# Kernel optimization log

Hardware: AMD Instinct MI355X
Metric: run time of the kernel (lower is better)

Reference implementation:

```python
import jax, jax.numpy as jnp
import numpy as np

N = 100000
E = 1600000
D_IN = 128
D_OUT = 128


def setup_inputs() -> dict:
    key = jax.random.key(0)
    k1, k2, k3, k4 = jax.random.split(key, 4)
    x = jax.random.normal(k1, (N, D_IN), dtype=jnp.float32)
    edge_index = jax.random.randint(k2, (2, E), 0, N, dtype=jnp.int64)
    edge_weight = jax.random.uniform(k3, (E,), dtype=jnp.float32)
    # PyG Linear (glorot) weight stored as [in, out] so that xw = x @ weight
    weight = jax.random.normal(k4, (D_IN, D_OUT), dtype=jnp.float32) * (1.0 / np.sqrt(D_IN))
    bias = jnp.zeros((D_OUT,), dtype=jnp.float32)
    prelu_a = jnp.full((1,), 0.25, dtype=jnp.float32)  # nn.PReLU default
    return {"x": x, "edge_index": edge_index, "edge_weight": edge_weight,
            "weight": weight, "bias": bias, "prelu_a": prelu_a}


def _gcn_forward(x, edge_index, edge_weight, weight, bias, prelu_a):
    n = x.shape[0]
    # Linear transform first (PyG GCNConv applies lin before propagate)
    xw = x @ weight  # [N, D_OUT]

    # gcn_norm: add self-loops with weight 1.0
    loop = jnp.arange(n, dtype=edge_index.dtype)
    row = jnp.concatenate([edge_index[0], loop])  # source
    col = jnp.concatenate([edge_index[1], loop])  # target
    ew = jnp.concatenate([edge_weight, jnp.ones((n,), dtype=edge_weight.dtype)])

    # symmetric normalization: deg computed at targets
    deg = jax.ops.segment_sum(ew, col, num_segments=n)  # [N]
    dinv = jnp.where(deg > 0, jax.lax.rsqrt(deg), 0.0)
    norm = dinv[row] * ew * dinv[col]  # [E+N]

    # gather-scale-scatter aggregation
    msgs = norm[:, None] * xw[row]  # [E+N, D_OUT]
    out = jax.ops.segment_sum(msgs, col, num_segments=n) + bias

    # PReLU (single shared slope)
    return jnp.where(out >= 0, out, prelu_a[0] * out)


def reference(x, edge_index, edge_weight, weight, bias, prelu_a):
    return _gcn_forward(x, edge_index, edge_weight, weight, bias, prelu_a)
```

## Files before the change

kernel.cpp:

```cpp
#include <hip/hip_runtime.h>
#include <hip/hip_bf16.h>

#define D 128
#define NBMAX 512
#define CURPAD 16

typedef __attribute__((ext_vector_type(8))) short bf16x8;
typedef __attribute__((ext_vector_type(4))) float f32x4;

__device__ inline unsigned short f2bf(float f) {
    unsigned u = __float_as_uint(f);
    u = (u + 0x7FFFu + ((u >> 16) & 1u)) >> 16;
    return (unsigned short)u;
}
__device__ inline float bf2f_lo(unsigned u) { return __uint_as_float(u << 16); }
__device__ inline float bf2f_hi(unsigned u) { return __uint_as_float(u & 0xFFFF0000u); }

__global__ void zero_int(int* __restrict__ p, int n) {
    int i = blockIdx.x * 256 + threadIdx.x;
    if (i < n) p[i] = 0;
}

__global__ __launch_bounds__(256) void bucket_count(const int* __restrict__ coli,
                                                    int* __restrict__ bcount, int NB, int E) {
    __shared__ int hist[NBMAX];
    int tid = threadIdx.x;
    for (int i = tid; i < NBMAX; i += 256) hist[i] = 0;
    __syncthreads();
    int base = blockIdx.x * 4096;
    #pragma unroll
    for (int j = 0; j < 16; ++j) {
        int e = base + j * 256 + tid;
        if (e < E) atomicAdd(&hist[coli[e] >> 8], 1);
    }
    __syncthreads();
    for (int i = tid; i < NB; i += 256) {
        int c = hist[i];
        if (c) atomicAdd(&bcount[i * CURPAD], c);
    }
}

__global__ __launch_bounds__(512) void bucket_scan(const int* __restrict__ bcount,
                                                   int* __restrict__ bbase,
                                                   int* __restrict__ bcursor, int NB) {
    __shared__ int sd[512];
    int tid = threadIdx.x;
    int v = (tid < NB) ? bcount[tid * CURPAD] : 0;
    sd[tid] = v; __syncthreads();
    for (int off = 1; off < 512; off <<= 1) {
        int t = (tid >= off) ? sd[tid - off] : 0;
        __syncthreads(); sd[tid] += t; __syncthreads();
    }
    int excl = sd[tid] - v;
    if (tid < NB) { bbase[tid] = excl; bcursor[tid * CURPAD] = excl; }
    if (tid == NB - 1) bbase[NB] = excl + v;
}

__global__ __launch_bounds__(1024) void phase1(const int* __restrict__ rowi,
                                               const int* __restrict__ coli,
                                               const float* __restrict__ ew,
                                               int* __restrict__ bcursor,
                                               int2* __restrict__ tmp, int E) {
    __shared__ int hist[NBMAX];
    __shared__ int runbase[NBMAX];
    int tid = threadIdx.x;
    for (int i = tid; i < NBMAX; i += 1024) hist[i] = 0;
    __syncthreads();
    int base = blockIdx.x * 8192;
    int col[8], row[8], rank[8]; float w[8];
    #pragma unroll
    for (int j = 0; j < 8; ++j) {
        int e = base + j * 1024 + tid;
        if (e < E) {
            col[j] = coli[e]; row[j] = rowi[e]; w[j] = ew[e];
            rank[j] = atomicAdd(&hist[col[j] >> 8], 1);
        }
    }
    __syncthreads();
    for (int i = tid; i < NBMAX; i += 1024) {
        int c = hist[i];
        runbase[i] = c ? atomicAdd(&bcursor[i * CURPAD], c) : 0;
    }
    __syncthreads();
    #pragma unroll
    for (int j = 0; j < 8; ++j) {
        int e = base + j * 1024 + tid;
        if (e < E) {
            int b = col[j] >> 8;
            int pos = runbase[b] + rank[j];
            tmp[pos] = make_int2(((col[j] & 255) << 24) | row[j], __float_as_int(w[j]));
        }
    }
}

__global__ __launch_bounds__(256) void phase2(const int2* __restrict__ tmp,
                                              const int* __restrict__ bbase,
                                              int* __restrict__ rowptr, int* __restrict__ cnt,
                                              float* __restrict__ dinv,
                                              int2* __restrict__ sorted, int N) {
    __shared__ unsigned int cnt_s[256];
    __shared__ unsigned long long deg_s[256];
    __shared__ int scan_s[256];
    __shared__ int cur[256];
    int tid = threadIdx.x;
    cnt_s[tid] = 0; deg_s[tid] = 0;
    __syncthreads();
    int start = bbase[blockIdx.x];
    int end   = bbase[blockIdx.x + 1];
    for (int e = start + tid; e < end; e += 256) {
        int2 v = tmp[e];
        unsigned coff = ((unsigned)v.x) >> 24;
        atomicAdd(&cnt_s[coff], 1u);
        unsigned long long fx =
            (unsigned long long)(__int_as_float(v.y) * 1048576.0f + 0.5f);
        atomicAdd(&deg_s[coff], fx);
    }
    __syncthreads();
    int v0 = (int)cnt_s[tid];
    scan_s[tid] = v0; __syncthreads();
    for (int off = 1; off < 256; off <<= 1) {
        int t = (tid >= off) ? scan_s[tid - off] : 0;
        __syncthreads(); scan_s[tid] += t; __syncthreads();
    }
    int excl = scan_s[tid] - v0;
    int node = blockIdx.x * 256 + tid;
    if (node < N) {
        rowptr[node] = start + excl;
        cnt[node] = v0;
        float deg = 1.0f + (float)((double)deg_s[tid] * (1.0 / 1048576.0));
        dinv[node] = rsqrtf(deg);
    }
    cur[tid] = start + excl;
    __syncthreads();
    for (int e = start + tid; e < end; e += 256) {
        int2 v = tmp[e];
        unsigned coff = ((unsigned)v.x) >> 24;
        int pos = atomicAdd(&cur[coff], 1);
        sorted[pos] = make_int2(v.x & 0xFFFFFF, v.y);
    }
}

__global__ __launch_bounds__(256) void gemm_mfma(const float* __restrict__ x,
                                                 const float* __restrict__ W,
                                                 unsigned short* __restrict__ xw, int N) {
    __shared__ bf16x8 smW[2048];
    int tid = threadIdx.x;

    for (int idx = tid; idx < 2048; idx += 256) {
        int tile = idx >> 6;
        int ln   = idx & 63;
        int kt   = tile >> 3;
        int ct   = tile & 7;
        int k0   = kt * 32 + (ln >> 4) * 8;
        int nn   = ct * 16 + (ln & 15);
        bf16x8 v;
        #pragma unroll
        for (int j = 0; j < 8; ++j) v[j] = (short)f2bf(W[(k0 + j) * D + nn]);
        smW[idx] = v;
    }
    __syncthreads();

    int wid  = tid >> 6;
    int lane = tid & 63;
    int quad = lane >> 4;
    int m16  = lane & 15;
    int row0 = blockIdx.x * 64 + wid * 16;
    int row  = row0 + m16;

    f32x4 acc[8];
    #pragma unroll
    for (int ct = 0; ct < 8; ++ct) acc[ct] = (f32x4){0.f, 0.f, 0.f, 0.f};

    #pragma unroll
    for (int kt = 0; kt < 4; ++kt) {
        bf16x8 a;
        if (row < N) {
            const float* xp = x + (size_t)row * D + kt * 32 + quad * 8;
            float4 u0 = *(const float4*)xp;
            float4 u1 = *(const float4*)(xp + 4);
            a[0] = (short)f2bf(u0.x); a[1] = (short)f2bf(u0.y);
            a[2] = (short)f2bf(u0.z); a[3] = (short)f2bf(u0.w);
            a[4] = (short)f2bf(u1.x); a[5] = (short)f2bf(u1.y);
            a[6] = (short)f2bf(u1.z); a[7] = (short)f2bf(u1.w);
        } else {
            #pragma unroll
            for (int j = 0; j < 8; ++j) a[j] = 0;
        }
        #pragma unroll
        for (int ct = 0; ct < 8; ++ct) {
            acc[ct] = __builtin_amdgcn_mfma_f32_16x16x32_bf16(
                a, smW[(kt * 8 + ct) * 64 + lane], acc[ct], 0, 0, 0);
        }
    }

    int rq = row0 + quad * 4;
    #pragma unroll
    for (int i = 0; i < 4; ++i) {
        int r = rq + i;
        if (r < N) {
            unsigned short* op = xw + (size_t)r * D + m16;
            #pragma unroll
            for (int ct = 0; ct < 8; ++ct) op[ct * 16] = f2bf(acc[ct][i]);
        }
    }
}

__global__ __launch_bounds__(256) void aggregate(const unsigned short* __restrict__ xw,
                                                 const float* __restrict__ dinv,
                                                 const int* __restrict__ rowptr,
                                                 const int* __restrict__ cnt,
                                                 const int2* __restrict__ sorted,
                                                 const float* __restrict__ bias,
                                                 const float* __restrict__ prelu_a,
                                                 float* __restrict__ out, int N) {
    int wid  = threadIdx.x >> 6;
    int lane = threadIdx.x & 63;
    int n = blockIdx.x * 4 + wid;
    if (n >= N) return;
    int d0 = lane * 2;
    float di = dinv[n];
    unsigned xs = *(const unsigned*)(xw + (size_t)n * D + d0);
    float ax = di * bf2f_lo(xs);
    float ay = di * bf2f_hi(xs);
    int s = rowptr[n];
    int cn = cnt[n];
    for (int base = 0; base < cn; base += 64) {
        int rem = cn - base;
        int m = rem < 64 ? rem : 64;
        int rsrc = 0; float wv = 0.f;
        if (lane < rem) {
            int2 er = sorted[s + base + lane];
            rsrc = er.x;
            wv = dinv[er.x] * __int_as_float(er.y);
        }
        int j = 0;
        for (; j + 4 <= m; j += 4) {
            int   r0 = __shfl(rsrc, j + 0), r1 = __shfl(rsrc, j + 1);
            int   r2 = __shfl(rsrc, j + 2), r3 = __shfl(rsrc, j + 3);
            float w0 = __shfl(wv, j + 0), w1 = __shfl(wv, j + 1);
            float w2 = __shfl(wv, j + 2), w3 = __shfl(wv, j + 3);
            unsigned v0 = *(const unsigned*)(xw + (size_t)r0 * D + d0);
            unsigned v1 = *(const unsigned*)(xw + (size_t)r1 * D + d0);
            unsigned v2 = *(const unsigned*)(xw + (size_t)r2 * D + d0);
            unsigned v3 = *(const unsigned*)(xw + (size_t)r3 * D + d0);
            ax = fmaf(w0, bf2f_lo(v0), ax); ay = fmaf(w0, bf2f_hi(v0), ay);
            ax = fmaf(w1, bf2f_lo(v1), ax); ay = fmaf(w1, bf2f_hi(v1), ay);
            ax = fmaf(w2, bf2f_lo(v2), ax); ay = fmaf(w2, bf2f_hi(v2), ay);
            ax = fmaf(w3, bf2f_lo(v3), ax); ay = fmaf(w3, bf2f_hi(v3), ay);
        }
        for (; j < m; ++j) {
            int   r = __shfl(rsrc, j);
            float w = __shfl(wv, j);
            unsigned v = *(const unsigned*)(xw + (size_t)r * D + d0);
            ax = fmaf(w, bf2f_lo(v), ax);
            ay = fmaf(w, bf2f_hi(v), ay);
        }
    }
    float a = prelu_a[0];
    float2 bv = *(const float2*)(bias + d0);
    float ox = fmaf(di, ax, bv.x);
    float oy = fmaf(di, ay, bv.y);
    ox = (ox >= 0.f) ? ox : a * ox;
    oy = (oy >= 0.f) ? oy : a * oy;
    *(float2*)(out + (size_t)n * D + d0) = make_float2(ox, oy);
}

extern "C" void kernel_launch(void* const* d_in, const int* in_sizes, int n_in,
                              void* d_out, int out_size, void* d_ws, size_t ws_size,
                              hipStream_t stream) {
    const float* x       = (const float*)d_in[0];
    const int*   ei      = (const int*)d_in[1];
    const float* ew      = (const float*)d_in[2];
    const float* W       = (const float*)d_in[3];
    const float* bias    = (const float*)d_in[4];
    const float* prelu_a = (const float*)d_in[5];
    float* out = (float*)d_out;

    int N = in_sizes[0] / D;
    int E = in_sizes[2];
    const int* rowi = ei;
    const int* coli = ei + E;
    int NB = (N + 255) >> 8;

    char* ws = (char*)d_ws;
    size_t o = 0;
    int2*  tmp    = (int2*)(ws + o); o += (size_t)E * 8;
    int2*  sorted = (int2*)(ws + o); o += (size_t)E * 8;
    unsigned short* xw = (unsigned short*)(ws + o); o += (size_t)N * D * 2;
    int* bcount  = (int*)(ws + o); o += (size_t)NB * CURPAD * 4;
    int* bcursor = (int*)(ws + o); o += (size_t)NB * CURPAD * 4;
    int* bbase   = (int*)(ws + o); o += ((size_t)NB + 1) * 4;
    o = (o + 255) & ~(size_t)255;
    int* rowptr  = (int*)(ws + o); o += (size_t)N * 4;
    int* cnt     = (int*)(ws + o); o += (size_t)N * 4;
    float* dinv  = (float*)(ws + o); o += (size_t)N * 4;

    zero_int<<<(NB * CURPAD + 255) / 256, 256, 0, stream>>>(bcount, NB * CURPAD);
    bucket_count<<<(E + 4095) / 4096, 256, 0, stream>>>(coli, bcount, NB, E);
    bucket_scan<<<1, 512, 0, stream>>>(bcount, bbase, bcursor, NB);
    phase1<<<(E + 8191) / 8192, 1024, 0, stream>>>(rowi, coli, ew, bcursor, tmp, E);
    phase2<<<NB, 256, 0, stream>>>(tmp, bbase, rowptr, cnt, dinv, sorted, N);
    gemm_mfma<<<(N + 63) / 64, 256, 0, stream>>>(x, W, xw, N);
    aggregate<<<(N + 3) / 4, 256, 0, stream>>>(xw, dinv, rowptr, cnt, sorted, bias, prelu_a, out, N);
}
```

Measured before the change: 246.8 us.

## Prescale xw by dinv in GEMM, vectorize aggregate gather across edge groups

The source-side dinv scaling moves into the GEMM epilogue, so the aggregate no longer does a per-edge dinv gather. The aggregate now has 16 lanes each load 16 bytes of a row, with four edges in flight per wavefront, a software-prefetched next load, and a cross-group shuffle reduction at the end. W is converted to bf16 MFMA layout once by a separate tiny kernel and read from global memory instead of being rebuilt in LDS by every GEMM block. The trade-offs are an extra reduction step, 48 of 64 lanes idle in the epilogue, and B-operand reads that now go through cache instead of LDS.

```diff
diff --git a/kernel.cpp b/kernel.cpp
--- a/kernel.cpp
+++ b/kernel.cpp
@@ -140,13 +140,10 @@
     }
 }
 
-__global__ __launch_bounds__(256) void gemm_mfma(const float* __restrict__ x,
-                                                 const float* __restrict__ W,
-                                                 unsigned short* __restrict__ xw, int N) {
-    __shared__ bf16x8 smW[2048];
-    int tid = threadIdx.x;
-
-    for (int idx = tid; idx < 2048; idx += 256) {
+__global__ __launch_bounds__(256) void prep_W(const float* __restrict__ W,
+                                              bf16x8* __restrict__ gW) {
+    int t = threadIdx.x;
+    for (int idx = t; idx < 2048; idx += 256) {
         int tile = idx >> 6;
         int ln   = idx & 63;
         int kt   = tile >> 3;
@@ -156,10 +153,15 @@
         bf16x8 v;
         #pragma unroll
         for (int j = 0; j < 8; ++j) v[j] = (short)f2bf(W[(k0 + j) * D + nn]);
-        smW[idx] = v;
-    }
-    __syncthreads();
-
+        gW[idx] = v;
+    }
+}
+
+__global__ __launch_bounds__(256) void gemm_mfma(const float* __restrict__ x,
+                                                 const bf16x8* __restrict__ gW,
+                                                 const float* __restrict__ dinv,
+                                                 unsigned short* __restrict__ yw, int N) {
+    int tid  = threadIdx.x;
     int wid  = tid >> 6;
     int lane = tid & 63;
     int quad = lane >> 4;
@@ -189,7 +191,7 @@
         #pragma unroll
         for (int ct = 0; ct < 8; ++ct) {
             acc[ct] = __builtin_amdgcn_mfma_f32_16x16x32_bf16(
-                a, smW[(kt * 8 + ct) * 64 + lane], acc[ct], 0, 0, 0);
+                a, gW[(kt * 8 + ct) * 64 + lane], acc[ct], 0, 0, 0);
         }
     }
 
@@ -198,14 +200,15 @@
     for (int i = 0; i < 4; ++i) {
         int r = rq + i;
         if (r < N) {
-            unsigned short* op = xw + (size_t)r * D + m16;
+            float sc = dinv[r];
+            unsigned short* op = yw + (size_t)r * D + m16;
             #pragma unroll
-            for (int ct = 0; ct < 8; ++ct) op[ct * 16] = f2bf(acc[ct][i]);
-        }
-    }
-}
-
-__global__ __launch_bounds__(256) void aggregate(const unsigned short* __restrict__ xw,
+            for (int ct = 0; ct < 8; ++ct) op[ct * 16] = f2bf(sc * acc[ct][i]);
+        }
+    }
+}
+
+__global__ __launch_bounds__(256) void aggregate(const unsigned short* __restrict__ yw,
                                                  const float* __restrict__ dinv,
                                                  const int* __restrict__ rowptr,
                                                  const int* __restrict__ cnt,
@@ -217,52 +220,74 @@
     int lane = threadIdx.x & 63;
     int n = blockIdx.x * 4 + wid;
     if (n >= N) return;
-    int d0 = lane * 2;
-    float di = dinv[n];
-    unsigned xs = *(const unsigned*)(xw + (size_t)n * D + d0);
-    float ax = di * bf2f_lo(xs);
-    float ay = di * bf2f_hi(xs);
+    int g = lane >> 4;
+    int l = lane & 15;
+    float2 a0 = {0.f,0.f}, a1 = {0.f,0.f}, a2 = {0.f,0.f}, a3 = {0.f,0.f};
     int s = rowptr[n];
     int cn = cnt[n];
     for (int base = 0; base < cn; base += 64) {
         int rem = cn - base;
         int m = rem < 64 ? rem : 64;
-        int rsrc = 0; float wv = 0.f;
-        if (lane < rem) {
-            int2 er = sorted[s + base + lane];
-            rsrc = er.x;
-            wv = dinv[er.x] * __int_as_float(er.y);
-        }
-        int j = 0;
-        for (; j + 4 <= m; j += 4) {
-            int   r0 = __shfl(rsrc, j + 0), r1 = __shfl(rsrc, j + 1);
-            int   r2 = __shfl(rsrc, j + 2), r3 = __shfl(rsrc, j + 3);
-            float w0 = __shfl(wv, j + 0), w1 = __shfl(wv, j + 1);
-            float w2 = __shfl(wv, j + 2), w3 = __shfl(wv, j + 3);
-            unsigned v0 = *(const unsigned*)(xw + (size_t)r0 * D + d0);
-            unsigned v1 = *(const unsigned*)(xw + (size_t)r1 * D + d0);
-            unsigned v2 = *(const unsigned*)(xw + (size_t)r2 * D + d0);
-            unsigned v3 = *(const unsigned*)(xw + (size_t)r3 * D + d0);
-            ax = fmaf(w0, bf2f_lo(v0), ax); ay = fmaf(w0, bf2f_hi(v0), ay);
-            ax = fmaf(w1, bf2f_lo(v1), ax); ay = fmaf(w1, bf2f_hi(v1), ay);
-            ax = fmaf(w2, bf2f_lo(v2), ax); ay = fmaf(w2, bf2f_hi(v2), ay);
-            ax = fmaf(w3, bf2f_lo(v3), ax); ay = fmaf(w3, bf2f_hi(v3), ay);
-        }
-        for (; j < m; ++j) {
-            int   r = __shfl(rsrc, j);
-            float w = __shfl(wv, j);
-            unsigned v = *(const unsigned*)(xw + (size_t)r * D + d0);
-            ax = fmaf(w, bf2f_lo(v), ax);
-            ay = fmaf(w, bf2f_hi(v), ay);
-        }
-    }
-    float a = prelu_a[0];
-    float2 bv = *(const float2*)(bias + d0);
-    float ox = fmaf(di, ax, bv.x);
-    float oy = fmaf(di, ay, bv.y);
-    ox = (ox >= 0.f) ? ox : a * ox;
-    oy = (oy >= 0.f) ? oy : a * oy;
-    *(float2*)(out + (size_t)n * D + d0) = make_float2(ox, oy);
+        int2 er = make_int2(0, 0);
+        if (lane < rem) er = sorted[s + base + lane];
+        float ewv = __int_as_float(er.y);
+        int idx = g;
+        int   r0 = __shfl(er.x, idx);
+        float w0 = __shfl(ewv, idx);
+        if (idx >= m) w0 = 0.f;
+        uint4 v0 = *(const uint4*)(yw + (size_t)r0 * D + l * 8);
+        for (int j = 4; j < m; j += 4) {
+            int idx1 = j + g;
+            int   r1 = __shfl(er.x, idx1);
+            float w1 = __shfl(ewv, idx1);
+            if (idx1 >= m) w1 = 0.f;
+            uint4 v1 = *(const uint4*)(yw + (size_t)r1 * D + l * 8);
+            a0.x = fmaf(w0, bf2f_lo(v0.x), a0.x); a0.y = fmaf(w0, bf2f_hi(v0.x), a0.y);
+            a1.x = fmaf(w0, bf2f_lo(v0.y), a1.x); a1.y = fmaf(w0, bf2f_hi(v0.y), a1.y);
+            a2.x = fmaf(w0, bf2f_lo(v0.z), a2.x); a2.y = fmaf(w0, bf2f_hi(v0.z), a2.y);
+            a3.x = fmaf(w0, bf2f_lo(v0.w), a3.x); a3.y = fmaf(w0, bf2f_hi(v0.w), a3.y);
+            v0 = v1; w0 = w1;
+        }
+        a0.x = fmaf(w0, bf2f_lo(v0.x), a0.x); a0.y = fmaf(w0, bf2f_hi(v0.x), a0.y);
+        a1.x = fmaf(w0, bf2f_lo(v0.y), a1.x); a1.y = fmaf(w0, bf2f_hi(v0.y), a1.y);
+        a2.x = fmaf(w0, bf2f_lo(v0.z), a2.x); a2.y = fmaf(w0, bf2f_hi(v0.z), a2.y);
+        a3.x = fmaf(w0, bf2f_lo(v0.w), a3.x); a3.y = fmaf(w0, bf2f_hi(v0.w), a3.y);
+    }
+    a0.x += __shfl_xor(a0.x, 16); a0.y += __shfl_xor(a0.y, 16);
+    a1.x += __shfl_xor(a1.x, 16); a1.y += __shfl_xor(a1.y, 16);
+    a2.x += __shfl_xor(a2.x, 16); a2.y += __shfl_xor(a2.y, 16);
+    a3.x += __shfl_xor(a3.x, 16); a3.y += __shfl_xor(a3.y, 16);
+    a0.x += __shfl_xor(a0.x, 32); a0.y += __shfl_xor(a0.y, 32);
+    a1.x += __shfl_xor(a1.x, 32); a1.y += __shfl_xor(a1.y, 32);
+    a2.x += __shfl_xor(a2.x, 32); a2.y += __shfl_xor(a2.y, 32);
+    a3.x += __shfl_xor(a3.x, 32); a3.y += __shfl_xor(a3.y, 32);
+
+    if (lane < 16) {
+        uint4 sv = *(const uint4*)(yw + (size_t)n * D + lane * 8);
+        a0.x += bf2f_lo(sv.x); a0.y += bf2f_hi(sv.x);
+        a1.x += bf2f_lo(sv.y); a1.y += bf2f_hi(sv.y);
+        a2.x += bf2f_lo(sv.z); a2.y += bf2f_hi(sv.z);
+        a3.x += bf2f_lo(sv.w); a3.y += bf2f_hi(sv.w);
+        float di = dinv[n];
+        float pa = prelu_a[0];
+        float4 b0 = *(const float4*)(bias + lane * 8);
+        float4 b1 = *(const float4*)(bias + lane * 8 + 4);
+        float4 o0, o1;
+        o0.x = fmaf(di, a0.x, b0.x); o0.y = fmaf(di, a0.y, b0.y);
+        o0.z = fmaf(di, a1.x, b0.z); o0.w = fmaf(di, a1.y, b0.w);
+        o1.x = fmaf(di, a2.x, b1.x); o1.y = fmaf(di, a2.y, b1.y);
+        o1.z = fmaf(di, a3.x, b1.z); o1.w = fmaf(di, a3.y, b1.w);
+        o0.x = (o0.x >= 0.f) ? o0.x : pa * o0.x;
+        o0.y = (o0.y >= 0.f) ? o0.y : pa * o0.y;
+        o0.z = (o0.z >= 0.f) ? o0.z : pa * o0.z;
+        o0.w = (o0.w >= 0.f) ? o0.w : pa * o0.w;
+        o1.x = (o1.x >= 0.f) ? o1.x : pa * o1.x;
+        o1.y = (o1.y >= 0.f) ? o1.y : pa * o1.y;
+        o1.z = (o1.z >= 0.f) ? o1.z : pa * o1.z;
+        o1.w = (o1.w >= 0.f) ? o1.w : pa * o1.w;
+        *(float4*)(out + (size_t)n * D + lane * 8)     = o0;
+        *(float4*)(out + (size_t)n * D + lane * 8 + 4) = o1;
+    }
 }
 
 extern "C" void kernel_launch(void* const* d_in, const int* in_sizes, int n_in,
@@ -286,7 +311,8 @@
     size_t o = 0;
     int2*  tmp    = (int2*)(ws + o); o += (size_t)E * 8;
     int2*  sorted = (int2*)(ws + o); o += (size_t)E * 8;
-    unsigned short* xw = (unsigned short*)(ws + o); o += (size_t)N * D * 2;
+    unsigned short* yw = (unsigned short*)(ws + o); o += (size_t)N * D * 2;
+    bf16x8* gW   = (bf16x8*)(ws + o); o += 2048 * 16;
     int* bcount  = (int*)(ws + o); o += (size_t)NB * CURPAD * 4;
     int* bcursor = (int*)(ws + o); o += (size_t)NB * CURPAD * 4;
     int* bbase   = (int*)(ws + o); o += ((size_t)NB + 1) * 4;
@@ -300,6 +326,7 @@
     bucket_scan<<<1, 512, 0, stream>>>(bcount, bbase, bcursor, NB);
     phase1<<<(E + 8191) / 8192, 1024, 0, stream>>>(rowi, coli, ew, bcursor, tmp, E);
     phase2<<<NB, 256, 0, stream>>>(tmp, bbase, rowptr, cnt, dinv, sorted, N);
-    gemm_mfma<<<(N + 63) / 64, 256, 0, stream>>>(x, W, xw, N);
-    aggregate<<<(N + 3) / 4, 256, 0, stream>>>(xw, dinv, rowptr, cnt, sorted, bias, prelu_a, out, N);
-}
+    prep_W<<<1, 256, 0, stream>>>(W, gW);
+    gemm_mfma<<<(N + 63) / 64, 256, 0, stream>>>(x, gW, dinv, yw, N);
+    aggregate<<<(N + 3) / 4, 256, 0, stream>>>(yw, dinv, rowptr, cnt, sorted, bias, prelu_a, out, N);
+}
```

Measured after the change: 251.5 us. Within noise of the previous version (+1.9%).
